# Kernel tuning notes

Hardware: AMD Instinct MI355X
Metric: run time of the kernel (lower is better)

The kernel has to match this reference:

```python
import jax, jax.numpy as jnp
import numpy as np

B, H, W = 2, 96, 96
IN, HID, P = 256, 10, 6
K = 9  # 3x3 taps
ADJ = np.array([
    [0,1,1,0,0,0],
    [1,0,0,1,0,0],
    [1,0,0,0,1,0],
    [0,1,0,0,0,1],
    [0,0,1,0,0,1],
    [0,0,0,1,1,0]])
EIDX = np.argwhere(ADJ)  # row-major, same order as torch.nonzero
E = EIDX.shape[0]


def _conv3x3(x, w, b):
    y = jax.lax.conv_general_dilated(x, w, (1, 1), ((1, 1), (1, 1)),
                                     dimension_numbers=('NCHW', 'OIHW', 'NCHW'))
    return y + b[None, :, None, None]


def _bilinear(x, ys, xs):
    # x [B,C,H,W]; ys,xs [B,K,H,W] float coords; zero padding outside image
    b, c, h, w = x.shape
    y0 = jnp.floor(ys); x0 = jnp.floor(xs)
    wy1 = ys - y0; wx1 = xs - x0
    xf = x.reshape(b, c, h * w)

    def gather(yc, xc):
        valid = ((yc >= 0) & (yc < h) & (xc >= 0) & (xc < w)).astype(x.dtype)
        yi = jnp.clip(yc, 0, h - 1).astype(jnp.int32)
        xi = jnp.clip(xc, 0, w - 1).astype(jnp.int32)
        idx = (yi * w + xi).reshape(b, -1)
        g = jax.vmap(lambda f, i: f[:, i])(xf, idx).reshape(b, c, *ys.shape[1:])
        return g * valid[:, None]

    return (gather(y0, x0) * ((1 - wy1) * (1 - wx1))[:, None]
            + gather(y0, x0 + 1) * ((1 - wy1) * wx1)[:, None]
            + gather(y0 + 1, x0) * (wy1 * (1 - wx1))[:, None]
            + gather(y0 + 1, x0 + 1) * (wy1 * wx1)[:, None])  # [B,C,K,H,W]


def _mdconv(x, off_w, off_b, w):
    # modulated deformable conv (DCNv2), 3x3, stride 1, pad 1, 1 deformable group
    b, c, h, wd = x.shape
    om = _conv3x3(x, off_w, off_b)           # [B, 27, H, W]
    off = om[:, :2 * K].reshape(b, K, 2, h, wd)   # (dy, dx) per tap
    mask = jax.nn.sigmoid(om[:, 2 * K:])          # [B, K, H, W]
    kh = (jnp.arange(K) // 3 - 1).astype(x.dtype)
    kw = (jnp.arange(K) % 3 - 1).astype(x.dtype)
    ys = jnp.arange(h, dtype=x.dtype)[None, None, :, None] + kh[None, :, None, None] + off[:, :, 0]
    xs = jnp.arange(wd, dtype=x.dtype)[None, None, None, :] + kw[None, :, None, None] + off[:, :, 1]
    s = _bilinear(x, ys, xs) * mask[:, None]      # [B,C,K,H,W]
    return jnp.einsum('bckhw,ock->bohw', s, w.reshape(w.shape[0], c, K))


def _bn4(x, g, b, eps=1e-5):  # BN over (N,H,W), x [B,C,H,W]
    m = x.mean((0, 2, 3), keepdims=True); v = x.var((0, 2, 3), keepdims=True)
    return g[None, :, None, None] * (x - m) * jax.lax.rsqrt(v + eps) + b[None, :, None, None]


def _bn5(x, g, b, eps=1e-5):  # x [P,B,C,H,W], per-part BN, g/b [P,C]
    m = x.mean((1, 3, 4), keepdims=True); v = x.var((1, 3, 4), keepdims=True)
    return g[:, None, :, None, None] * (x - m) * jax.lax.rsqrt(v + eps) + b[:, None, :, None, None]


def _part_dep(pA, pB, o1w, o1b, d1w, g1, b1, o2w, o2b, d2w, g2, b2, o_w, o_b, a_w, a_b):
    x = jnp.concatenate([pA, pB], axis=1)  # [B, 2*HID, H, W]
    x = jax.nn.relu(_bn4(_mdconv(x, o1w, o1b, d1w), g1, b1))
    x = jax.nn.relu(_bn4(_mdconv(x, o2w, o2b, d2w), g2, b2))
    ab_att = jax.nn.sigmoid(jnp.einsum('bchw,oc->bohw', x, o_w) + o_b[None, :, None, None])
    a_att = jax.nn.sigmoid(jnp.einsum('bchw,oc->bohw', pA, a_w) + a_b[None, :, None, None])
    return ab_att * (1 - a_att)  # [B,1,H,W]


def _forward(p_fea, xp, xh, att_w, att_b, du_w, du_b, dl_w, dl_b,
             upd_w, upd_g, upd_b,
             off1_w, off1_b, dcn1_w, bn1_g, bn1_b,
             off2_w, off2_b, dcn2_w, bn2_g, bn2_b,
             out_w, out_b, aatt_w, aatt_b, edge_src, edge_dst):
    # grouped 1x1 self-attention over concatenated part features
    self_att = jax.nn.sigmoid(jnp.einsum('gbchw,gc->gbhw', xp, att_w)
                              + att_b[:, None, None, None])  # [P,B,H,W]
    # edge-wise deformable message passing: gather endpoints, vmap over edges
    pA = xp[edge_src]  # [E,B,HID,H,W]
    pB = xp[edge_dst]
    msgs = jax.vmap(_part_dep)(pA, pB, off1_w, off1_b, dcn1_w, bn1_g, bn1_b,
                               off2_w, off2_b, dcn2_w, bn2_g, bn2_b,
                               out_w, out_b, aatt_w, aatt_b)  # [E,B,1,H,W]
    xpp = jax.ops.segment_sum(msgs, edge_dst, num_segments=P)  # [P,B,1,H,W]
    # half-body decomposition gates
    d_u = jax.nn.sigmoid(jnp.einsum('bchw,oc->bohw', xh[0], du_w) + du_b[None, :, None, None])
    d_l = jax.nn.sigmoid(jnp.einsum('bchw,oc->bohw', xh[1], dl_w) + dl_b[None, :, None, None])
    decomp = jnp.stack([d_u, d_u, d_u, d_u, d_l, d_l], 0)  # upper parts 1-4, lower 5-6
    gate = 1.0 + decomp + self_att[:, :, None] + xpp  # [P,B,1,H,W]
    z = p_fea[None] * gate                            # [P,B,IN,H,W]
    y = jnp.einsum('gbchw,goc->gbohw', z, upd_w)      # [P,B,HID,H,W]
    return jax.nn.relu(_bn5(y, upd_g, upd_b))


def setup_inputs() -> dict:
    k = jax.random.split(jax.random.key(0), 16)
    n = jax.random.normal
    f = jnp.float32
    return {
        'p_fea': n(k[0], (B, IN, H, W), f),
        'xp': n(k[1], (P, B, HID, H, W), f),
        'xh': n(k[2], (2, B, HID, H, W), f),
        'att_w': n(k[3], (P, HID), f) * 0.3, 'att_b': jnp.zeros((P,), f),
        'du_w': n(k[4], (1, HID), f) * 0.3, 'du_b': jnp.zeros((1,), f),
        'dl_w': n(k[5], (1, HID), f) * 0.3, 'dl_b': jnp.zeros((1,), f),
        'upd_w': n(k[6], (P, HID, IN), f) * 0.06,
        'upd_g': jnp.ones((P, HID), f), 'upd_b': jnp.zeros((P, HID), f),
        'off1_w': n(k[7], (E, 27, 2 * HID, 3, 3), f) * 0.01, 'off1_b': jnp.zeros((E, 27), f),
        'dcn1_w': n(k[8], (E, 2 * HID, 2 * HID, 3, 3), f) * 0.07,
        'bn1_g': jnp.ones((E, 2 * HID), f), 'bn1_b': jnp.zeros((E, 2 * HID), f),
        'off2_w': n(k[9], (E, 27, 2 * HID, 3, 3), f) * 0.01, 'off2_b': jnp.zeros((E, 27), f),
        'dcn2_w': n(k[10], (E, HID, 2 * HID, 3, 3), f) * 0.07,
        'bn2_g': jnp.ones((E, HID), f), 'bn2_b': jnp.zeros((E, HID), f),
        'out_w': n(k[11], (E, 1, HID), f) * 0.3, 'out_b': jnp.zeros((E, 1), f),
        'aatt_w': n(k[12], (E, 1, HID), f) * 0.3, 'aatt_b': jnp.zeros((E, 1), f),
        'edge_src': jnp.asarray(EIDX[:, 0], jnp.int32),
        'edge_dst': jnp.asarray(EIDX[:, 1], jnp.int32),
    }


def reference(p_fea, xp, xh, att_w, att_b, du_w, du_b, dl_w, dl_b,
              upd_w, upd_g, upd_b,
              off1_w, off1_b, dcn1_w, bn1_g, bn1_b,
              off2_w, off2_b, dcn2_w, bn2_g, bn2_b,
              out_w, out_b, aatt_w, aatt_b, edge_src, edge_dst):
    return _forward(p_fea, xp, xh, att_w, att_b, du_w, du_b, dl_w, dl_b,
                    upd_w, upd_g, upd_b,
                    off1_w, off1_b, dcn1_w, bn1_g, bn1_b,
                    off2_w, off2_b, dcn2_w, bn2_g, bn2_b,
                    out_w, out_b, aatt_w, aatt_b, edge_src, edge_dst)
```

## Files before the change

kernel.cpp:

```cpp
#include <hip/hip_runtime.h>
#include <hip/hip_bf16.h>


#define NE 12
#define NPART 6
#define BB 2
#define HH 96
#define WW 96
#define HWD (HH*WW)
#define CIN2 20
#define NHID 10
#define NIN 256

#define BOX 20
#define BCOL 21
#define NPIX (BOX*BCOL)
#define GHALF (NPIX*8)
#define SROW 40

typedef __attribute__((ext_vector_type(8))) short s16x8;
typedef __attribute__((ext_vector_type(4))) float f32x4;

__device__ __forceinline__ float sigf(float x) { return 1.f / (1.f + __expf(-x)); }
__device__ __forceinline__ float bfbits2f(unsigned int u) {
    return __uint_as_float(u << 16);
}
__device__ __forceinline__ unsigned short f2bfbits(float v) {
    __hip_bfloat16 h = __float2bfloat16(v);
    return *reinterpret_cast<unsigned short*>(&h);
}
__device__ __forceinline__ void wave_lds_fence() {
    asm volatile("s_waitcnt lgkmcnt(0)" ::: "memory");
    __builtin_amdgcn_sched_barrier(0);
}

__global__ __launch_bounds__(256)
void xpose_weights(const float* __restrict__ off1_w, const float* __restrict__ off1_b,
                   const float* __restrict__ dcn1_w,
                   const float* __restrict__ off2_w, const float* __restrict__ off2_b,
                   const float* __restrict__ dcn2_w,
                   const float* __restrict__ upd_w,
                   unsigned short* __restrict__ bf1, float* __restrict__ o1b,
                   unsigned short* __restrict__ ws1,
                   unsigned short* __restrict__ bf2, float* __restrict__ o2b,
                   unsigned short* __restrict__ ws2,
                   float* __restrict__ uwt)
{
    int idx = blockIdx.x * 256 + threadIdx.x;
    if (idx < 110592) {
        int e = idx / 9216, r = idx % 9216;
        int t = r / 1024, r2 = r % 1024;
        int nt = r2 / 512, r3 = r2 % 512;
        int lane = r3 / 8, i = r3 % 8;
        int k = (lane >> 4)*8 + i;
        int col = nt*16 + (lane & 15);
        float v = (k < CIN2 && col < 27) ? off1_w[((e*27 + col)*CIN2 + k)*9 + t] : 0.f;
        bf1[idx] = f2bfbits(v);
        return;
    }
    idx -= 110592;
    if (idx < 324) { o1b[idx] = off1_b[idx]; return; }
    idx -= 324;
    if (idx < 110592) {
        int e = idx / 9216, r = idx % 9216;
        int t = r / 1024, r2 = r % 1024;
        int nt = r2 / 512, r3 = r2 % 512;
        int lane = r3 / 8, i = r3 % 8;
        int c = (lane >> 4)*8 + i;
        int o = nt*16 + (lane & 15);
        float v = (c < CIN2 && o < CIN2) ? dcn1_w[((e*20 + o)*CIN2 + c)*9 + t] : 0.f;
        ws1[idx] = f2bfbits(v);
        return;
    }
    idx -= 110592;
    if (idx < 110592) {
        int e = idx / 9216, r = idx % 9216;
        int t = r / 1024, r2 = r % 1024;
        int nt = r2 / 512, r3 = r2 % 512;
        int lane = r3 / 8, i = r3 % 8;
        int k = (lane >> 4)*8 + i;
        int col = nt*16 + (lane & 15);
        float v = (k < CIN2 && col < 27) ? off2_w[((e*27 + col)*CIN2 + k)*9 + t] : 0.f;
        bf2[idx] = f2bfbits(v);
        return;
    }
    idx -= 110592;
    if (idx < 324) { o2b[idx] = off2_b[idx]; return; }
    idx -= 324;
    if (idx < 55296) {
        int e = idx / 4608, r = idx % 4608;
        int t = r / 512, r3 = r % 512;
        int lane = r3 / 8, i = r3 % 8;
        int c = (lane >> 4)*8 + i;
        int o = lane & 15;
        float v = (c < CIN2 && o < NHID) ? dcn2_w[((e*10 + o)*CIN2 + c)*9 + t] : 0.f;
        ws2[idx] = f2bfbits(v);
        return;
    }
    idx -= 55296;
    if (idx < 15360) {
        int p = idx / 2560, r = idx % 2560, c = r / 10, o = r % 10;
        uwt[idx] = upd_w[(p*10 + o)*256 + c];
        return;
    }
}

template<int COUT, bool L1>
__global__ __launch_bounds__(256, 4)
void dcn_tiled(const float* __restrict__ xin_all,
               const float* __restrict__ xp,
               const int* __restrict__ esrc, const int* __restrict__ edst,
               const unsigned short* __restrict__ bfr_all,
               const float* __restrict__ bo_all,
               const unsigned short* __restrict__ ws_all,
               const float* __restrict__ bnS, const float* __restrict__ bnT,
               float* __restrict__ out)
{
    constexpr int NT = (COUT > 16) ? 2 : 1;
    const int b = blockIdx.y, e = blockIdx.z;
    const int ty0 = (blockIdx.x / 6) * 16, tx0 = (blockIdx.x % 6) * 16;
    const int tid = threadIdx.x;
    const int ly = tid >> 4, lx = tid & 15;
    const int h = ty0 + ly, w = tx0 + lx;
    const int r0 = ty0 - 2, c0 = tx0 - 2;

    const float* __restrict__ xin = xin_all + (size_t)(e*BB + b)*CIN2*HWD;
    const float* __restrict__ bo  = bo_all + e*27;
    const unsigned short* __restrict__ bfr = bfr_all + (size_t)e*9216;
    const unsigned short* __restrict__ wsf = ws_all + (size_t)e*(9*NT*512);

    __shared__ unsigned short ldsb[3*GHALF];
    __shared__ unsigned short stile[256*SROW];

    #pragma unroll 1
    for (int i = tid; i < 3*NPIX; i += 256) {
        int g = i / NPIX;
        int pix = i - g*NPIX;
        int rr = pix / BCOL, cc = pix - rr*BCOL;
        int y = r0 + rr, x = c0 + cc;
        bool inb = (y >= 0 && y < HH && x >= 0 && x < WW);
        int hw = y*WW + x;
        unsigned int dpk[4];
        #pragma unroll
        for (int jj = 0; jj < 4; jj++) {
            unsigned int packed = 0;
            #pragma unroll
            for (int hl = 0; hl < 2; hl++) {
                int c = g*8 + jj*2 + hl;
                float v = 0.f;
                if (inb && c < CIN2) {
                    if (L1) {
                        int part = (c < NHID) ? esrc[e] : edst[e];
                        int ch   = (c < NHID) ? c : c - NHID;
                        v = xp[((size_t)(part*BB + b)*NHID + ch)*HWD + hw];
                    } else {
                        v = xin[(size_t)c*HWD + hw];
                        v = fmaxf(fmaf(v, bnS[e*CIN2 + c], bnT[e*CIN2 + c]), 0.f);
                    }
                }
                packed |= ((unsigned int)f2bfbits(v)) << (16*hl);
            }
            dpk[jj] = packed;
        }
        *reinterpret_cast<uint4*>(&ldsb[g*GHALF + pix*8]) =
            make_uint4(dpk[0], dpk[1], dpk[2], dpk[3]);
    }
    __syncthreads();

    const int lane = tid & 63;
    const int wv   = tid >> 6;
    const int lrow = lane & 15;
    const int lkg  = lane >> 4;

    {
        const int gsel = (lkg < 3) ? lkg : 2;
        f32x4 cacc[4][2];
        #pragma unroll
        for (int mt = 0; mt < 4; mt++)
            #pragma unroll
            for (int nt = 0; nt < 2; nt++)
                cacc[mt][nt] = f32x4{0.f, 0.f, 0.f, 0.f};

        const s16x8* ap = reinterpret_cast<const s16x8*>(&ldsb[gsel*GHALF]);
        #pragma unroll 1
        for (int t = 0; t < 9; t++) {
            const s16x8* bp = reinterpret_cast<const s16x8*>(bfr + t*1024);
            s16x8 b0 = bp[lane];
            s16x8 b1 = bp[64 + lane];
            int dty = t/3 - 1, dtx = t - (t/3)*3 - 1;
            #pragma unroll
            for (int mt = 0; mt < 4; mt++) {
                int pxl = wv*64 + mt*16 + lrow;
                int pix = ((pxl >> 4) + 2 + dty)*BCOL + ((pxl & 15) + 2 + dtx);
                s16x8 a = ap[pix];
                cacc[mt][0] = __builtin_amdgcn_mfma_f32_16x16x32_bf16(a, b0, cacc[mt][0], 0, 0, 0);
                cacc[mt][1] = __builtin_amdgcn_mfma_f32_16x16x32_bf16(a, b1, cacc[mt][1], 0, 0, 0);
            }
        }
        #pragma unroll
        for (int mt = 0; mt < 4; mt++)
            #pragma unroll
            for (int nt = 0; nt < 2; nt++)
                #pragma unroll
                for (int r = 0; r < 4; r++) {
                    int row = wv*64 + mt*16 + lkg*4 + r;
                    stile[row*SROW + nt*16 + lrow] = f2bfbits(cacc[mt][nt][r]);
                }
    }
    wave_lds_fence();

    float om[27];
    {
        const uint4* orow = reinterpret_cast<const uint4*>(&stile[(size_t)tid*SROW]);
        uint4 u0 = orow[0], u1 = orow[1], u2 = orow[2], u3 = orow[3];
        unsigned int dwv[14] = {u0.x,u0.y,u0.z,u0.w, u1.x,u1.y,u1.z,u1.w,
                                u2.x,u2.y,u2.z,u2.w, u3.x,u3.y};
        #pragma unroll
        for (int o = 0; o < 27; o++) {
            unsigned int bits = (o & 1) ? (dwv[o>>1] >> 16) : (dwv[o>>1] & 0xffffu);
            om[o] = bfbits2f(bits) + bo[o];
        }
    }
    {
        unsigned short* mr = &stile[(size_t)tid*SROW];
        *reinterpret_cast<uint2*>(mr + 20) = make_uint2(0u, 0u);
        *reinterpret_cast<uint2*>(mr + 24) = make_uint2(0u, 0u);
        *reinterpret_cast<uint2*>(mr + 28) = make_uint2(0u, 0u);
    }

    f32x4 sacc[4][NT];
    #pragma unroll
    for (int mt = 0; mt < 4; mt++)
        #pragma unroll
        for (int nt = 0; nt < NT; nt++)
            sacc[mt][nt] = f32x4{0.f, 0.f, 0.f, 0.f};

    #pragma unroll
    for (int k = 0; k < 9; k++) {
        float m  = sigf(om[18 + k]);
        float ys = (float)(h + k/3 - 1) + om[2*k];
        float xs = (float)(w + k%3 - 1) + om[2*k + 1];
        float y0f = floorf(ys), x0f = floorf(xs);
        int iy = (int)y0f, ix = (int)x0f;
        float fy = ys - y0f, fx = xs - x0f;
        bool vy0 = (iy >= 0) && (iy < HH);
        bool vy1 = (iy >= -1) && (iy < HH-1);
        bool vx0 = (ix >= 0) && (ix < WW);
        bool vx1 = (ix >= -1) && (ix < WW-1);
        float w00 = (vy0 && vx0) ? (1.f-fy)*(1.f-fx)*m : 0.f;
        float w01 = (vy0 && vx1) ? (1.f-fy)*fx*m       : 0.f;
        float w10 = (vy1 && vx0) ? fy*(1.f-fx)*m       : 0.f;
        float w11 = (vy1 && vx1) ? fy*fx*m             : 0.f;
        int cy0 = min(max(iy,   0), HH-1), cy1 = min(max(iy+1, 0), HH-1);
        int cx0 = min(max(ix,   0), WW-1), cx1 = min(max(ix+1, 0), WW-1);

        unsigned int pk[10];
        bool staged = (cy0 >= r0) && (cy1 <= r0 + BOX-1) &&
                      (cx0 >= c0) && (cx1 <= c0 + BOX-1);
        if (staged) {
            const int p00 = (cy0-r0)*BCOL + (cx0-c0);
            const int p01 = (cy0-r0)*BCOL + (cx1-c0);
            const int p10 = (cy1-r0)*BCOL + (cx0-c0);
            const int p11 = (cy1-r0)*BCOL + (cx1-c0);
            #pragma unroll
            for (int g = 0; g < 3; g++) {
                const s16x8* gp = reinterpret_cast<const s16x8*>(&ldsb[g*GHALF]);
                s16x8 a8 = gp[p00], b8 = gp[p01], c8 = gp[p10], d8 = gp[p11];
                #pragma unroll
                for (int jp = 0; jp < 4; jp++) {
                    if (g*8 + jp*2 < CIN2) {
                        float s0, s1;
                        {
                            int j = jp*2;
                            float av = bfbits2f((unsigned short)a8[j]);
                            float bv = bfbits2f((unsigned short)b8[j]);
                            float cv = bfbits2f((unsigned short)c8[j]);
                            float dv = bfbits2f((unsigned short)d8[j]);
                            s0 = w00*av + w01*bv + w10*cv + w11*dv;
                        }
                        {
                            int j = jp*2 + 1;
                            float av = bfbits2f((unsigned short)a8[j]);
                            float bv = bfbits2f((unsigned short)b8[j]);
                            float cv = bfbits2f((unsigned short)c8[j]);
                            float dv = bfbits2f((unsigned short)d8[j]);
                            s1 = w00*av + w01*bv + w10*cv + w11*dv;
                        }
                        pk[g*4 + jp] = (unsigned int)f2bfbits(s0)
                                     | ((unsigned int)f2bfbits(s1) << 16);
                    }
                }
            }
        } else {
            int o00 = cy0*WW + cx0, o01 = cy0*WW + cx1;
            int o10 = cy1*WW + cx0, o11 = cy1*WW + cx1;
            float sv[20];
            #pragma unroll
            for (int c = 0; c < CIN2; c++) {
                const float* src;
                float sc = 1.f, sh = 0.f;
                if (L1) {
                    int part = (c < NHID) ? esrc[e] : edst[e];
                    int ch   = (c < NHID) ? c : c - NHID;
                    src = xp + ((size_t)(part*BB + b)*NHID + ch)*HWD;
                } else {
                    src = xin + (size_t)c*HWD;
                    sc = bnS[e*CIN2 + c]; sh = bnT[e*CIN2 + c];
                }
                float av = src[o00], bv = src[o01], cv = src[o10], dv = src[o11];
                if (!L1) {
                    av = fmaxf(fmaf(av, sc, sh), 0.f); bv = fmaxf(fmaf(bv, sc, sh), 0.f);
                    cv = fmaxf(fmaf(cv, sc, sh), 0.f); dv = fmaxf(fmaf(dv, sc, sh), 0.f);
                }
                sv[c] = w00*av + w01*bv + w10*cv + w11*dv;
            }
            #pragma unroll
            for (int jp = 0; jp < 10; jp++)
                pk[jp] = (unsigned int)f2bfbits(sv[2*jp])
                       | ((unsigned int)f2bfbits(sv[2*jp+1]) << 16);
        }

        {
            unsigned short* mr = &stile[(size_t)tid*SROW];
            *reinterpret_cast<uint4*>(mr)      = make_uint4(pk[0], pk[1], pk[2], pk[3]);
            *reinterpret_cast<uint4*>(mr + 8)  = make_uint4(pk[4], pk[5], pk[6], pk[7]);
            *reinterpret_cast<uint2*>(mr + 16) = make_uint2(pk[8], pk[9]);
        }
        wave_lds_fence();

        {
            const s16x8* wsp = reinterpret_cast<const s16x8*>(wsf + (size_t)k*NT*512);
            s16x8 wb0 = wsp[lane];
            s16x8 wb1{};
            if constexpr (NT == 2) wb1 = wsp[64 + lane];
            #pragma unroll
            for (int mt = 0; mt < 4; mt++) {
                int pxl = wv*64 + mt*16 + lrow;
                s16x8 a = *reinterpret_cast<const s16x8*>(&stile[pxl*SROW + lkg*8]);
                sacc[mt][0] = __builtin_amdgcn_mfma_f32_16x16x32_bf16(a, wb0, sacc[mt][0], 0, 0, 0);
                if constexpr (NT == 2)
                    sacc[mt][1] = __builtin_amdgcn_mfma_f32_16x16x32_bf16(a, wb1, sacc[mt][1], 0, 0, 0);
            }
        }
        wave_lds_fence();
    }

    {
        float* ldsf = reinterpret_cast<float*>(stile) + wv*1280;
        #pragma unroll
        for (int mt = 0; mt < 4; mt++) {
            #pragma unroll
            for (int nt = 0; nt < NT; nt++) {
                int o = nt*16 + lrow;
                if (o < COUT) {
                    #pragma unroll
                    for (int r = 0; r < 4; r++) {
                        int lp = mt*16 + lkg*4 + r;
                        ldsf[o*64 + lp] = sacc[mt][nt][r];
                    }
                }
            }
        }
        wave_lds_fence();
        float* op = out + (size_t)(e*BB + b)*COUT*HWD + h*WW + w;
        #pragma unroll
        for (int o = 0; o < COUT; o++)
            op[(size_t)o*HWD] = ldsf[o*64 + (tid & 63)];
    }
}

__device__ __forceinline__ void bn_finish(float s1, float s2, int n, float g, float bt,
                                          float* scale, float* shift, int idx)
{
    float mean = s1 / (float)n;
    float var  = fmaxf(s2 / (float)n - mean*mean, 0.f);
    float rs   = rsqrtf(var + 1e-5f);
    scale[idx] = g * rs;
    shift[idx] = bt - mean * g * rs;
}

template<int C>
__global__ __launch_bounds__(256)
void bn_stats_flat(const float* __restrict__ x, const float* __restrict__ gamma,
                   const float* __restrict__ beta, float* __restrict__ scale,
                   float* __restrict__ shift)
{
    const int gc = blockIdx.x;
    const int g = gc / C, c = gc % C;
    const int N = BB * HWD;
    float s1 = 0.f, s2 = 0.f;
    for (int idx = threadIdx.x; idx < N; idx += 256) {
        int b = idx / HWD, p = idx % HWD;
        float v = x[((size_t)(g*BB + b)*C + c)*HWD + p];
        s1 += v; s2 += v*v;
    }
    __shared__ float r1[256], r2[256];
    r1[threadIdx.x] = s1; r2[threadIdx.x] = s2;
    __syncthreads();
    for (int s = 128; s > 0; s >>= 1) {
        if (threadIdx.x < s) { r1[threadIdx.x] += r1[threadIdx.x+s]; r2[threadIdx.x] += r2[threadIdx.x+s]; }
        __syncthreads();
    }
    if (threadIdx.x == 0)
        bn_finish(r1[0], r2[0], N, gamma[gc], beta[gc], scale, shift, gc);
}

__global__ __launch_bounds__(256)
void mgq_kernel(const float* __restrict__ t2all, const float* __restrict__ s2,
                const float* __restrict__ sh2, const float* __restrict__ o_w,
                const float* __restrict__ o_b, const float* __restrict__ a_w,
                const float* __restrict__ a_b, const float* __restrict__ xp,
                const float* __restrict__ xh,
                const float* __restrict__ att_w, const float* __restrict__ att_b,
                const float* __restrict__ du_w, const float* __restrict__ du_b,
                const float* __restrict__ dl_w, const float* __restrict__ dl_b,
                const int* __restrict__ esrc, const int* __restrict__ edst,
                const float* __restrict__ p_fea, const float* __restrict__ wq_all,
                float* __restrict__ y)
{
    int px = blockIdx.x * 256 + threadIdx.x;
    int b = blockIdx.y, p = blockIdx.z;

    float s = att_b[p];
    #pragma unroll
    for (int c = 0; c < NHID; c++)
        s += xp[((size_t)(p*BB + b)*NHID + c)*HWD + px] * att_w[p*NHID + c];
    float satt = sigf(s);

    int hs = (p < 4) ? 0 : 1;
    const float* dw = (p < 4) ? du_w : dl_w;
    float d = (p < 4) ? du_b[0] : dl_b[0];
    #pragma unroll
    for (int c = 0; c < NHID; c++)
        d += xh[((size_t)(hs*BB + b)*NHID + c)*HWD + px] * dw[c];
    float dec = sigf(d);

    float xpp = 0.f;
    for (int e = 0; e < NE; e++) {
        if (edst[e] != p) continue;
        float sab = o_b[e];
        #pragma unroll
        for (int c = 0; c < NHID; c++) {
            float v = t2all[((size_t)(e*BB + b)*NHID + c)*HWD + px];
            v = fmaxf(fmaf(v, s2[e*NHID+c], sh2[e*NHID+c]), 0.f);
            sab += v * o_w[e*NHID + c];
        }
        int sp = esrc[e];
        float sa = a_b[e];
        #pragma unroll
        for (int c = 0; c < NHID; c++)
            sa += xp[((size_t)(sp*BB + b)*NHID + c)*HWD + px] * a_w[e*NHID + c];
        xpp += sigf(sab) * (1.f - sigf(sa));
    }
    float gate = 1.f + dec + satt + xpp;

    const float* wq = wq_all + (size_t)p*NIN*NHID;
    const float* pf = p_fea + (size_t)b*NIN*HWD + px;
    float acc[NHID];
    #pragma unroll
    for (int o = 0; o < NHID; o++) acc[o] = 0.f;
    for (int c = 0; c < NIN; c += 8) {
        float v0 = pf[(size_t)(c+0)*HWD];
        float v1 = pf[(size_t)(c+1)*HWD];
        float v2 = pf[(size_t)(c+2)*HWD];
        float v3 = pf[(size_t)(c+3)*HWD];
        float v4 = pf[(size_t)(c+4)*HWD];
        float v5 = pf[(size_t)(c+5)*HWD];
        float v6 = pf[(size_t)(c+6)*HWD];
        float v7 = pf[(size_t)(c+7)*HWD];
        const float* wc = wq + c*NHID;
        #pragma unroll
        for (int o = 0; o < NHID; o++) acc[o] = fmaf(v0, wc[o], acc[o]);
        #pragma unroll
        for (int o = 0; o < NHID; o++) acc[o] = fmaf(v1, wc[NHID + o], acc[o]);
        #pragma unroll
        for (int o = 0; o < NHID; o++) acc[o] = fmaf(v2, wc[2*NHID + o], acc[o]);
        #pragma unroll
        for (int o = 0; o < NHID; o++) acc[o] = fmaf(v3, wc[3*NHID + o], acc[o]);
        #pragma unroll
        for (int o = 0; o < NHID; o++) acc[o] = fmaf(v4, wc[4*NHID + o], acc[o]);
        #pragma unroll
        for (int o = 0; o < NHID; o++) acc[o] = fmaf(v5, wc[5*NHID + o], acc[o]);
        #pragma unroll
        for (int o = 0; o < NHID; o++) acc[o] = fmaf(v6, wc[6*NHID + o], acc[o]);
        #pragma unroll
        for (int o = 0; o < NHID; o++) acc[o] = fmaf(v7, wc[7*NHID + o], acc[o]);
    }
    float* yp = y + ((size_t)(p*BB + b)*NHID)*HWD + px;
    #pragma unroll
    for (int o = 0; o < NHID; o++) yp[(size_t)o*HWD] = acc[o] * gate;
}

__global__ __launch_bounds__(256)
void out_kernel(const float* __restrict__ y, const float* __restrict__ s5,
                const float* __restrict__ t5, float* __restrict__ out)
{
    int px = blockIdx.x * 256 + threadIdx.x;
    int bo = blockIdx.y, p = blockIdx.z;
    int b = bo / NHID, o = bo % NHID;
    size_t idx = ((size_t)(p*BB + b)*NHID + o)*HWD + px;
    out[idx] = fmaxf(fmaf(y[idx], s5[p*NHID+o], t5[p*NHID+o]), 0.f);
}

extern "C" void kernel_launch(void* const* d_in, const int* in_sizes, int n_in,
                              void* d_out, int out_size, void* d_ws, size_t ws_size,
                              hipStream_t stream)
{
    (void)in_sizes; (void)n_in; (void)out_size; (void)ws_size;

    const float* p_fea  = (const float*)d_in[0];
    const float* xp     = (const float*)d_in[1];
    const float* xh     = (const float*)d_in[2];
    const float* att_w  = (const float*)d_in[3];
    const float* att_b  = (const float*)d_in[4];
    const float* du_w   = (const float*)d_in[5];
    const float* du_b   = (const float*)d_in[6];
    const float* dl_w   = (const float*)d_in[7];
    const float* dl_b   = (const float*)d_in[8];
    const float* upd_w  = (const float*)d_in[9];
    const float* upd_g  = (const float*)d_in[10];
    const float* upd_b  = (const float*)d_in[11];
    const float* off1_w = (const float*)d_in[12];
    const float* off1_b = (const float*)d_in[13];
    const float* dcn1_w = (const float*)d_in[14];
    const float* bn1_g  = (const float*)d_in[15];
    const float* bn1_b  = (const float*)d_in[16];
    const float* off2_w = (const float*)d_in[17];
    const float* off2_b = (const float*)d_in[18];
    const float* dcn2_w = (const float*)d_in[19];
    const float* bn2_g  = (const float*)d_in[20];
    const float* bn2_b  = (const float*)d_in[21];
    const float* out_w  = (const float*)d_in[22];
    const float* out_b  = (const float*)d_in[23];
    const float* aatt_w = (const float*)d_in[24];
    const float* aatt_b = (const float*)d_in[25];
    const int* esrc     = (const int*)d_in[26];
    const int* edst     = (const int*)d_in[27];
    float* outp = (float*)d_out;
    float* ws = (float*)d_ws;

    constexpr size_t o_x1   = 0;
    constexpr size_t o_t2   = o_x1  + (size_t)NE*BB*CIN2*HWD;
    constexpr size_t o_bf1  = o_t2  + (size_t)NE*BB*NHID*HWD;
    constexpr size_t o_b1   = o_bf1 + 55296;
    constexpr size_t o_ws1  = o_b1  + 324;
    constexpr size_t o_bf2  = o_ws1 + 55296;
    constexpr size_t o_b2   = o_bf2 + 55296;
    constexpr size_t o_ws2  = o_b2  + 324;
    constexpr size_t o_uw   = o_ws2 + 27648;
    constexpr size_t o_bn1s = o_uw  + 15360;
    constexpr size_t o_bn1t = o_bn1s + NE*CIN2;
    constexpr size_t o_bn2s = o_bn1t + NE*CIN2;
    constexpr size_t o_bn2t = o_bn2s + NE*NHID;
    constexpr size_t o_bn5s = o_bn2t + NE*NHID;
    constexpr size_t o_bn5t = o_bn5s + NPART*NHID;
    constexpr size_t o_y    = o_bn5t + NPART*NHID;
    float* x1 = ws + o_x1;
    float* t2 = ws + o_t2;
    float* y  = ws + o_y;
    unsigned short* bf1 = (unsigned short*)(ws + o_bf1);
    unsigned short* ws1 = (unsigned short*)(ws + o_ws1);
    unsigned short* bf2 = (unsigned short*)(ws + o_bf2);
    unsigned short* ws2 = (unsigned short*)(ws + o_ws2);

    xpose_weights<<<dim3(1575), 256, 0, stream>>>(
        off1_w, off1_b, dcn1_w, off2_w, off2_b, dcn2_w, upd_w,
        bf1, ws+o_b1, ws1, bf2, ws+o_b2, ws2, ws+o_uw);

    dcn_tiled<CIN2, true><<<dim3(36, BB, NE), 256, 0, stream>>>(
        nullptr, xp, esrc, edst, bf1, ws+o_b1, ws1,
        nullptr, nullptr, x1);

    bn_stats_flat<CIN2><<<dim3(NE*CIN2), 256, 0, stream>>>(
        x1, bn1_g, bn1_b, ws+o_bn1s, ws+o_bn1t);

    dcn_tiled<NHID, false><<<dim3(36, BB, NE), 256, 0, stream>>>(
        x1, nullptr, esrc, edst, bf2, ws+o_b2, ws2,
        ws+o_bn1s, ws+o_bn1t, t2);

    bn_stats_flat<NHID><<<dim3(NE*NHID), 256, 0, stream>>>(
        t2, bn2_g, bn2_b, ws+o_bn2s, ws+o_bn2t);

    mgq_kernel<<<dim3(36, BB, NPART), 256, 0, stream>>>(
        t2, ws+o_bn2s, ws+o_bn2t, out_w, out_b, aatt_w, aatt_b, xp, xh,
        att_w, att_b, du_w, du_b, dl_w, dl_b, esrc, edst,
        p_fea, ws+o_uw, y);

    bn_stats_flat<NHID><<<dim3(NPART*NHID), 256, 0, stream>>>(
        y, upd_g, upd_b, ws+o_bn5s, ws+o_bn5t);

    out_kernel<<<dim3(36, BB*NHID, NPART), 256, 0, stream>>>(
        y, ws+o_bn5s, ws+o_bn5t, outp);
}
```

Measured before the change: 191.2 us.

## Fuse BatchNorm statistics into producer kernels via atomic accumulation

Removes the three separate bn_stats_flat reduction passes that re-read x1, t2 and y from global memory. The DCN and mgq kernels now reduce per-channel sum and sum of squares in registers and wave shuffles, then atomically add them to zeroed workspace buffers. Tiny single-block finalize kernels convert these to scale/shift. This adds atomic contention and makes the float accumulation order nondeterministic. It also relies on xpose_weights zeroing the stats buffers on every call.

```diff
diff --git a/kernel.cpp b/kernel.cpp
--- a/kernel.cpp
+++ b/kernel.cpp
@@ -44,7 +44,7 @@
                    unsigned short* __restrict__ ws1,
                    unsigned short* __restrict__ bf2, float* __restrict__ o2b,
                    unsigned short* __restrict__ ws2,
-                   float* __restrict__ uwt)
+                   float* __restrict__ uwt, float* __restrict__ zstats)
 {
     int idx = blockIdx.x * 256 + threadIdx.x;
     if (idx < 110592) {
@@ -103,6 +103,27 @@
         uwt[idx] = upd_w[(p*10 + o)*256 + c];
         return;
     }
+    idx -= 15360;
+    if (idx < 840) { zstats[idx] = 0.f; return; }
+}
+
+__device__ __forceinline__ void bn_finish(float s1, float s2, int n, float g, float bt,
+                                          float* scale, float* shift, int idx)
+{
+    float mean = s1 / (float)n;
+    float var  = fmaxf(s2 / (float)n - mean*mean, 0.f);
+    float rs   = rsqrtf(var + 1e-5f);
+    scale[idx] = g * rs;
+    shift[idx] = bt - mean * g * rs;
+}
+
+__global__ __launch_bounds__(256)
+void bn_finalize(const float* __restrict__ sum, const float* __restrict__ sq,
+                 const float* __restrict__ gamma, const float* __restrict__ beta,
+                 float* __restrict__ scale, float* __restrict__ shift, int n)
+{
+    int i = threadIdx.x;
+    if (i < n) bn_finish(sum[i], sq[i], BB*HWD, gamma[i], beta[i], scale, shift, i);
 }
 
 template<int COUT, bool L1>
@@ -114,7 +135,8 @@
                const float* __restrict__ bo_all,
                const unsigned short* __restrict__ ws_all,
                const float* __restrict__ bnS, const float* __restrict__ bnT,
-               float* __restrict__ out)
+               float* __restrict__ out,
+               float* __restrict__ statSum, float* __restrict__ statSq)
 {
     constexpr int NT = (COUT > 16) ? 2 : 1;
     const int b = blockIdx.y, e = blockIdx.z;
@@ -345,6 +367,25 @@
         wave_lds_fence();
     }
 
+    #pragma unroll
+    for (int nt = 0; nt < NT; nt++) {
+        int o = nt*16 + lrow;
+        float ls = 0.f, lq = 0.f;
+        #pragma unroll
+        for (int mt = 0; mt < 4; mt++)
+            #pragma unroll
+            for (int r = 0; r < 4; r++) {
+                float v = sacc[mt][nt][r];
+                ls += v; lq += v*v;
+            }
+        ls += __shfl_xor(ls, 16); lq += __shfl_xor(lq, 16);
+        ls += __shfl_xor(ls, 32); lq += __shfl_xor(lq, 32);
+        if (lkg == 0 && o < COUT) {
+            atomicAdd(&statSum[e*COUT + o], ls);
+            atomicAdd(&statSq[e*COUT + o], lq);
+        }
+    }
+
     {
         float* ldsf = reinterpret_cast<float*>(stile) + wv*1280;
         #pragma unroll
@@ -367,42 +408,6 @@
         for (int o = 0; o < COUT; o++)
             op[(size_t)o*HWD] = ldsf[o*64 + (tid & 63)];
     }
-}
-
-__device__ __forceinline__ void bn_finish(float s1, float s2, int n, float g, float bt,
-                                          float* scale, float* shift, int idx)
-{
-    float mean = s1 / (float)n;
-    float var  = fmaxf(s2 / (float)n - mean*mean, 0.f);
-    float rs   = rsqrtf(var + 1e-5f);
-    scale[idx] = g * rs;
-    shift[idx] = bt - mean * g * rs;
-}
-
-template<int C>
-__global__ __launch_bounds__(256)
-void bn_stats_flat(const float* __restrict__ x, const float* __restrict__ gamma,
-                   const float* __restrict__ beta, float* __restrict__ scale,
-                   float* __restrict__ shift)
-{
-    const int gc = blockIdx.x;
-    const int g = gc / C, c = gc % C;
-    const int N = BB * HWD;
-    float s1 = 0.f, s2 = 0.f;
-    for (int idx = threadIdx.x; idx < N; idx += 256) {
-        int b = idx / HWD, p = idx % HWD;
-        float v = x[((size_t)(g*BB + b)*C + c)*HWD + p];
-        s1 += v; s2 += v*v;
-    }
-    __shared__ float r1[256], r2[256];
-    r1[threadIdx.x] = s1; r2[threadIdx.x] = s2;
-    __syncthreads();
-    for (int s = 128; s > 0; s >>= 1) {
-        if (threadIdx.x < s) { r1[threadIdx.x] += r1[threadIdx.x+s]; r2[threadIdx.x] += r2[threadIdx.x+s]; }
-        __syncthreads();
-    }
-    if (threadIdx.x == 0)
-        bn_finish(r1[0], r2[0], N, gamma[gc], beta[gc], scale, shift, gc);
 }
 
 __global__ __launch_bounds__(256)
@@ -416,7 +421,8 @@
                 const float* __restrict__ dl_w, const float* __restrict__ dl_b,
                 const int* __restrict__ esrc, const int* __restrict__ edst,
                 const float* __restrict__ p_fea, const float* __restrict__ wq_all,
-                float* __restrict__ y)
+                float* __restrict__ y,
+                float* __restrict__ s5sum, float* __restrict__ s5sq)
 {
     int px = blockIdx.x * 256 + threadIdx.x;
     int b = blockIdx.y, p = blockIdx.z;
@@ -488,7 +494,21 @@
     }
     float* yp = y + ((size_t)(p*BB + b)*NHID)*HWD + px;
     #pragma unroll
-    for (int o = 0; o < NHID; o++) yp[(size_t)o*HWD] = acc[o] * gate;
+    for (int o = 0; o < NHID; o++) {
+        float v = acc[o] * gate;
+        yp[(size_t)o*HWD] = v;
+        float ls = v, lq = v*v;
+        ls += __shfl_xor(ls, 1);  lq += __shfl_xor(lq, 1);
+        ls += __shfl_xor(ls, 2);  lq += __shfl_xor(lq, 2);
+        ls += __shfl_xor(ls, 4);  lq += __shfl_xor(lq, 4);
+        ls += __shfl_xor(ls, 8);  lq += __shfl_xor(lq, 8);
+        ls += __shfl_xor(ls, 16); lq += __shfl_xor(lq, 16);
+        ls += __shfl_xor(ls, 32); lq += __shfl_xor(lq, 32);
+        if ((threadIdx.x & 63) == 0) {
+            atomicAdd(&s5sum[p*NHID + o], ls);
+            atomicAdd(&s5sq[p*NHID + o], lq);
+        }
+    }
 }
 
 __global__ __launch_bounds__(256)
@@ -554,7 +574,14 @@
     constexpr size_t o_bn2t = o_bn2s + NE*NHID;
     constexpr size_t o_bn5s = o_bn2t + NE*NHID;
     constexpr size_t o_bn5t = o_bn5s + NPART*NHID;
-    constexpr size_t o_y    = o_bn5t + NPART*NHID;
+    constexpr size_t o_st   = o_bn5t + NPART*NHID;
+    constexpr size_t o_s1u  = o_st;
+    constexpr size_t o_s1q  = o_s1u + 240;
+    constexpr size_t o_s2u  = o_s1q + 240;
+    constexpr size_t o_s2q  = o_s2u + 120;
+    constexpr size_t o_s5u  = o_s2q + 120;
+    constexpr size_t o_s5q  = o_s5u + 60;
+    constexpr size_t o_y    = o_s5q + 60;
     float* x1 = ws + o_x1;
     float* t2 = ws + o_t2;
     float* y  = ws + o_y;
@@ -563,31 +590,31 @@
     unsigned short* bf2 = (unsigned short*)(ws + o_bf2);
     unsigned short* ws2 = (unsigned short*)(ws + o_ws2);
 
-    xpose_weights<<<dim3(1575), 256, 0, stream>>>(
+    xpose_weights<<<dim3(1578), 256, 0, stream>>>(
         off1_w, off1_b, dcn1_w, off2_w, off2_b, dcn2_w, upd_w,
-        bf1, ws+o_b1, ws1, bf2, ws+o_b2, ws2, ws+o_uw);
+        bf1, ws+o_b1, ws1, bf2, ws+o_b2, ws2, ws+o_uw, ws+o_st);
 
     dcn_tiled<CIN2, true><<<dim3(36, BB, NE), 256, 0, stream>>>(
         nullptr, xp, esrc, edst, bf1, ws+o_b1, ws1,
-        nullptr, nullptr, x1);
-
-    bn_stats_flat<CIN2><<<dim3(NE*CIN2), 256, 0, stream>>>(
-        x1, bn1_g, bn1_b, ws+o_bn1s, ws+o_bn1t);
+        nullptr, nullptr, x1, ws+o_s1u, ws+o_s1q);
+
+    bn_finalize<<<dim3(1), 256, 0, stream>>>(
+        ws+o_s1u, ws+o_s1q, bn1_g, bn1_b, ws+o_bn1s, ws+o_bn1t, NE*CIN2);
 
     dcn_tiled<NHID, false><<<dim3(36, BB, NE), 256, 0, stream>>>(
         x1, nullptr, esrc, edst, bf2, ws+o_b2, ws2,
-        ws+o_bn1s, ws+o_bn1t, t2);
-
-    bn_stats_flat<NHID><<<dim3(NE*NHID), 256, 0, stream>>>(
-        t2, bn2_g, bn2_b, ws+o_bn2s, ws+o_bn2t);
+        ws+o_bn1s, ws+o_bn1t, t2, ws+o_s2u, ws+o_s2q);
+
+    bn_finalize<<<dim3(1), 256, 0, stream>>>(
+        ws+o_s2u, ws+o_s2q, bn2_g, bn2_b, ws+o_bn2s, ws+o_bn2t, NE*NHID);
 
     mgq_kernel<<<dim3(36, BB, NPART), 256, 0, stream>>>(
         t2, ws+o_bn2s, ws+o_bn2t, out_w, out_b, aatt_w, aatt_b, xp, xh,
         att_w, att_b, du_w, du_b, dl_w, dl_b, esrc, edst,
-        p_fea, ws+o_uw, y);
-
-    bn_stats_flat<NHID><<<dim3(NPART*NHID), 256, 0, stream>>>(
-        y, upd_g, upd_b, ws+o_bn5s, ws+o_bn5t);
+        p_fea, ws+o_uw, y, ws+o_s5u, ws+o_s5q);
+
+    bn_finalize<<<dim3(1), 256, 0, stream>>>(
+        ws+o_s5u, ws+o_s5q, upd_g, upd_b, ws+o_bn5s, ws+o_bn5t, NPART*NHID);
 
     out_kernel<<<dim3(36, BB*NHID, NPART), 256, 0, stream>>>(
         y, ws+o_bn5s, ws+o_bn5t, outp);
```

New measurement: 274.6 us. 43.6% more time.
